# Kernel optimization log

Measured on AMD Instinct MI355X. Metric: run time of the kernel, lower is better.

Reference implementation:

```python
import jax, jax.numpy as jnp
import numpy as np

N = 50000
E = 800000
IN_C = 128
HID = 32
HEADS = 4
G = 512      # number of graphs in batch
OUT_C = 100
NEG_SLOPE = 0.2
EPS = 1e-16


def _gat_params(key, f_in, heads, c):
    k1, k2, k3, k4 = jax.random.split(key, 4)
    s = 1.0 / np.sqrt(f_in)
    return {
        'W': jax.random.uniform(k1, (heads * c, f_in), jnp.float32, -s, s),
        'att_src': jax.random.normal(k2, (heads, c), jnp.float32) * 0.1,
        'att_dst': jax.random.normal(k3, (heads, c), jnp.float32) * 0.1,
        'b': jnp.zeros((heads * c,), jnp.float32),
    }


def setup_inputs() -> dict:
    key = jax.random.key(0)
    ks = jax.random.split(key, 8)
    x = jax.random.normal(ks[0], (N, IN_C), jnp.float32)
    edge_index = jax.random.randint(ks[1], (2, E), 0, N, jnp.int64)
    batch = jnp.sort(jax.random.randint(ks[2], (N,), 0, G, jnp.int64))
    p1 = _gat_params(ks[3], IN_C, HEADS, HID)
    p2 = _gat_params(ks[4], HEADS * HID, HEADS, HID)
    p3 = _gat_params(ks[5], HEADS * HID, HEADS, HID)
    s = 1.0 / np.sqrt(HEADS * HID)
    fc_W = jax.random.uniform(ks[6], (OUT_C, HEADS * HID), jnp.float32, -s, s)
    fc_b = jnp.zeros((OUT_C,), jnp.float32)
    return {
        'x': x, 'edge_index': edge_index, 'batch': batch,
        'W1': p1['W'], 'as1': p1['att_src'], 'ad1': p1['att_dst'], 'b1': p1['b'],
        'W2': p2['W'], 'as2': p2['att_src'], 'ad2': p2['att_dst'], 'b2': p2['b'],
        'W3': p3['W'], 'as3': p3['att_src'], 'ad3': p3['att_dst'], 'b3': p3['b'],
        'fc_W': fc_W, 'fc_b': fc_b,
    }


def gat_conv(x, src, dst, W, att_src, att_dst, b):
    # x: [N, F_in] -> h: [N, H, C]
    h = (x @ W.T).reshape(N, HEADS, HID)
    a_src = jnp.einsum('nhc,hc->nh', h, att_src)   # [N, H]
    a_dst = jnp.einsum('nhc,hc->nh', h, att_dst)
    alpha = a_src[src] + a_dst[dst]                 # [E', H]
    alpha = jax.nn.leaky_relu(alpha, NEG_SLOPE)
    # segment softmax over incoming edges of each dst node
    m = jax.ops.segment_max(alpha, dst, num_segments=N)
    alpha = jnp.exp(alpha - m[dst])
    denom = jax.ops.segment_sum(alpha, dst, num_segments=N)
    alpha = alpha / (denom[dst] + EPS)
    msg = alpha[:, :, None] * h[src]                # [E', H, C]
    out = jax.ops.segment_sum(msg, dst, num_segments=N)
    return out.reshape(N, HEADS * HID) + b


def reference(x, edge_index, batch,
              W1, as1, ad1, b1, W2, as2, ad2, b2, W3, as3, ad3, b3,
              fc_W, fc_b):
    # add self loops (PyG GATConv default)
    loops = jnp.arange(N, dtype=edge_index.dtype)
    src = jnp.concatenate([edge_index[0], loops])
    dst = jnp.concatenate([edge_index[1], loops])
    h = jax.nn.elu(gat_conv(x, src, dst, W1, as1, ad1, b1))
    h = jax.nn.elu(gat_conv(h, src, dst, W2, as2, ad2, b2))
    h = jax.nn.elu(gat_conv(h, src, dst, W3, as3, ad3, b3))
    # global mean pool over graphs
    sums = jax.ops.segment_sum(h, batch, num_segments=G)        # [G, H*C]
    cnts = jax.ops.segment_sum(jnp.ones((N,), h.dtype), batch, num_segments=G)
    pooled = sums / jnp.maximum(cnts, 1.0)[:, None]
    # dropout p=0.5 is identity in eval mode
    return pooled @ fc_W.T + fc_b
```

## Files before the change

### kernel.cpp

```cpp
#include <hip/hip_runtime.h>
#include <math.h>

#define NN 50000
#define EE 800000
#define GG 512
#define OUTC 100
#define NEG 0.2f
#define STRIDE 64
#define SCAT_BLOCKS 782

typedef __attribute__((ext_vector_type(8))) short bf16x8;
typedef __attribute__((ext_vector_type(8))) short s16x8;
typedef __attribute__((ext_vector_type(8))) unsigned short us8;
typedef __attribute__((ext_vector_type(4))) float f32x4;

__device__ inline ushort f2bf(float v) {
  unsigned u = __float_as_uint(v);
  unsigned r = (u + 0x7fff + ((u >> 16) & 1)) >> 16;
  return (ushort)r;
}

__global__ __launch_bounds__(256) void k_scatter_prep(const int* __restrict__ ei,
    int* __restrict__ cursor, ushort* __restrict__ srcs,
    const float* __restrict__ W0, const float* __restrict__ W1, const float* __restrict__ W2,
    const float* __restrict__ as0, const float* __restrict__ as1, const float* __restrict__ as2,
    const float* __restrict__ ad0, const float* __restrict__ ad1, const float* __restrict__ ad2,
    ushort* __restrict__ hi, ushort* __restrict__ lo) {
  if (blockIdx.x < SCAT_BLOCKS) {
    int base = blockIdx.x << 10;
#pragma unroll
    for (int t = 0; t < 4; ++t) {
      int e = base + (t << 8) + threadIdx.x;
      if (e < EE) {
        int d = ei[EE + e];
        int s = ei[e];
        int pos = atomicAdd(&cursor[d], 1);
        if (pos < STRIDE) srcs[(d << 6) + pos] = (ushort)s;
      }
    }
  } else {
    int pb = blockIdx.x - SCAT_BLOCKS;
    int layer = pb / 68, bx = pb % 68;
    const float* W  = (layer == 0) ? W0 : (layer == 1) ? W1 : W2;
    const float* av = (layer == 0) ? as0 : (layer == 1) ? as1 : as2;
    const float* dv = (layer == 0) ? ad0 : (layer == 1) ? ad1 : ad2;
    ushort* hiL = hi + (size_t)layer * 144 * 128;
    ushort* loL = lo + (size_t)layer * 144 * 128;
    int idx = bx * 256 + threadIdx.x;
    if (bx < 64) {
      float v = W[idx];
      ushort hb = f2bf(v);
      float hf = __uint_as_float(((unsigned)hb) << 16);
      hiL[idx] = hb;
      loL[idx] = f2bf(v - hf);
    } else {
      int j2 = idx - 64 * 256;
      int j = j2 >> 7, k = j2 & 127;
      int head = j & 3;
      const float* vec = (j < 4) ? &av[head * 32] : &dv[head * 32];
      float dot = 0.f;
#pragma unroll
      for (int c = 0; c < 32; c++) dot += W[(head * 32 + c) * 128 + k] * vec[c];
      ushort hb = f2bf(dot);
      float hf = __uint_as_float(((unsigned)hb) << 16);
      hiL[(128 + j) * 128 + k] = hb;
      loL[(128 + j) * 128 + k] = f2bf(dot - hf);
      hiL[(136 + j) * 128 + k] = 0;
      loL[(136 + j) * 128 + k] = 0;
    }
  }
}

template <bool TAIL>
__device__ __forceinline__ void gemm_core(const float* __restrict__ feat,
    const ushort* __restrict__ Whi, const ushort* __restrict__ Wlo,
    short* __restrict__ hq, float* __restrict__ asp,
    float* __restrict__ adstf, int n0, int t) {
  int wave = t >> 6, lane = t & 63;
  int quad = lane >> 4, r16 = lane & 15;

  f32x4 acc[2][9];
#pragma unroll
  for (int mt = 0; mt < 2; mt++)
#pragma unroll
    for (int nt = 0; nt < 9; nt++) acc[mt][nt] = (f32x4)0.f;

#pragma unroll
  for (int ks = 0; ks < 4; ks++) {
    bf16x8 ah[2], al[2];
#pragma unroll
    for (int mt = 0; mt < 2; mt++) {
      int row = n0 + wave * 32 + mt * 16 + r16;
      float4 va, vb;
      if (TAIL && row >= NN) {
        va = make_float4(0.f, 0.f, 0.f, 0.f); vb = va;
      } else {
        const float4* fp = (const float4*)&feat[(size_t)row * 128 + ks * 32 + quad * 8];
        va = fp[0]; vb = fp[1];
      }
      float vv[8] = {va.x, va.y, va.z, va.w, vb.x, vb.y, vb.z, vb.w};
      us8 hh, ll;
#pragma unroll
      for (int j = 0; j < 8; j++) {
        ushort hb = f2bf(vv[j]);
        float hf = __uint_as_float(((unsigned)hb) << 16);
        hh[j] = hb;
        ll[j] = (ushort)(__float_as_uint(vv[j] - hf) >> 16);
      }
      ah[mt] = (bf16x8)hh;
      al[mt] = (bf16x8)ll;
    }
#pragma unroll
    for (int nt = 0; nt < 9; nt++) {
      int wrow = (nt < 8) ? (nt * 16 + r16) : (128 + r16);
      size_t wo = (size_t)wrow * 128 + ks * 32 + quad * 8;
      bf16x8 bh = *(const bf16x8*)&Whi[wo];
      bf16x8 bl = *(const bf16x8*)&Wlo[wo];
#pragma unroll
      for (int mt = 0; mt < 2; mt++) {
        acc[mt][nt] = __builtin_amdgcn_mfma_f32_16x16x32_bf16(ah[mt], bh, acc[mt][nt], 0, 0, 0);
        acc[mt][nt] = __builtin_amdgcn_mfma_f32_16x16x32_bf16(al[mt], bh, acc[mt][nt], 0, 0, 0);
        acc[mt][nt] = __builtin_amdgcn_mfma_f32_16x16x32_bf16(ah[mt], bl, acc[mt][nt], 0, 0, 0);
      }
    }
  }

#pragma unroll
  for (int mt = 0; mt < 2; mt++) {
#pragma unroll
    for (int reg = 0; reg < 4; reg++) {
      float am = 0.f;
#pragma unroll
      for (int nt = 0; nt < 8; nt++) am = fmaxf(am, fabsf(acc[mt][nt][reg]));
#pragma unroll
      for (int off = 1; off < 16; off <<= 1) am = fmaxf(am, __shfl_xor(am, off));
      int node = n0 + wave * 32 + mt * 16 + quad * 4 + reg;
      if (!TAIL || node < NN) {
        float amc = fmaxf(am, 1e-20f);
        float rq = 32767.f / amc;
        if (r16 < 4) asp[node * 8 + r16] = acc[mt][8][reg];
        else if (r16 < 8) adstf[node * 4 + r16 - 4] = acc[mt][8][reg];
        else if (r16 == 8) asp[node * 8 + 4] = amc * (1.f / 32767.f);
        short* dq = &hq[(size_t)node * 128 + r16];
#pragma unroll
        for (int nt = 0; nt < 8; nt++)
          dq[nt * 16] = (short)__float2int_rn(acc[mt][nt][reg] * rq);
      }
    }
  }
}

__global__ __launch_bounds__(256) void k_gemm_mfma(const float* __restrict__ feat,
    const ushort* __restrict__ Whi, const ushort* __restrict__ Wlo,
    short* __restrict__ hq, float* __restrict__ asp,
    float* __restrict__ adstf) {
  int n0 = blockIdx.x * 128;
  if (n0 + 128 <= NN)
    gemm_core<false>(feat, Whi, Wlo, hq, asp, adstf, n0, threadIdx.x);
  else
    gemm_core<true>(feat, Whi, Wlo, hq, asp, adstf, n0, threadIdx.x);
}

__global__ __launch_bounds__(256) void k_gather(const short* __restrict__ hq,
    const float* __restrict__ asp,
    const float4* __restrict__ adst,
    const int* __restrict__ cursor, const ushort* __restrict__ srcs,
    const float* __restrict__ bias, float* __restrict__ outf) {
  __shared__ alignas(16) int   s_src[2][4][4][16];
  __shared__ alignas(16) float s_wt[2][4][4][4][20];

  int wave = threadIdx.x >> 6, lane = threadIdx.x & 63;
  int grp = lane >> 4;
  int gl = lane & 15;
  int node = blockIdx.x * 16 + wave * 4 + grp;
  int head = gl >> 2;
  int c0 = gl << 3;

  int deg = 0, e0 = 0;
  float4 ad = make_float4(0.f, 0.f, 0.f, 0.f);
  if (node < NN) {
    deg = min(cursor[node], STRIDE);
    e0 = node << 6;
    ad = adst[node];
  }
  int rounds = (deg + 15) >> 4;

  float acc[8];
#pragma unroll
  for (int i = 0; i < 8; i++) acc[i] = 0.f;
  float ws0 = 0.f, ws1 = 0.f, ws2 = 0.f, ws3 = 0.f;
  float wself = 0.f;

  int nsn = 0, nlive = 0;

  auto phase1 = [&](int r) {
    int j = (r << 4) + gl;
    nlive = (j < deg);
    nsn = nlive ? (int)srcs[e0 + j] : 0;
  };

  auto phase2 = [&](int b) {
    float q0 = 0.f, q1 = 0.f, q2 = 0.f, q3 = 0.f;
    if (nlive) {
      const float4 a = *(const float4*)&asp[nsn * 8];
      float sc = asp[nsn * 8 + 4];
      float v, w0, w1, w2, w3;
      v = a.x + ad.x; v = v > 0.f ? v : NEG * v; w0 = __expf(v);
      v = a.y + ad.y; v = v > 0.f ? v : NEG * v; w1 = __expf(v);
      v = a.z + ad.z; v = v > 0.f ? v : NEG * v; w2 = __expf(v);
      v = a.w + ad.w; v = v > 0.f ? v : NEG * v; w3 = __expf(v);
      ws0 += w0; ws1 += w1; ws2 += w2; ws3 += w3;
      q0 = w0 * sc; q1 = w1 * sc; q2 = w2 * sc; q3 = w3 * sc;
    }
    s_src[b][wave][grp][gl] = nsn << 7;
    s_wt[b][wave][grp][0][gl] = q0;
    s_wt[b][wave][grp][1][gl] = q1;
    s_wt[b][wave][grp][2][gl] = q2;
    s_wt[b][wave][grp][3][gl] = q3;
  };

  auto consume = [&](int r, int b) {
    int cnt = deg - (r << 4);
    cnt = min(cnt, 16);
    const int* srow = &s_src[b][wave][grp][0];
    const float* wrow = &s_wt[b][wave][grp][head][0];
#pragma unroll
    for (int c = 0; c < 2; ++c) {
      int k0 = c << 3;
      if (k0 < cnt) {
        int4 sa = *(const int4*)&srow[k0];
        int4 sb = *(const int4*)&srow[k0 + 4];
        float4 wa = *(const float4*)&wrow[k0];
        float4 wb = *(const float4*)&wrow[k0 + 4];
        s16x8 qa = *(const s16x8*)&hq[sa.x + c0];
        s16x8 qb = *(const s16x8*)&hq[sa.y + c0];
        s16x8 qc = *(const s16x8*)&hq[sa.z + c0];
        s16x8 qd = *(const s16x8*)&hq[sa.w + c0];
        s16x8 qe = *(const s16x8*)&hq[sb.x + c0];
        s16x8 qf = *(const s16x8*)&hq[sb.y + c0];
        s16x8 qg = *(const s16x8*)&hq[sb.z + c0];
        s16x8 qh = *(const s16x8*)&hq[sb.w + c0];
#pragma unroll
        for (int i = 0; i < 8; i++) acc[i] = fmaf(wa.x, (float)qa[i], acc[i]);
#pragma unroll
        for (int i = 0; i < 8; i++) acc[i] = fmaf(wa.y, (float)qb[i], acc[i]);
#pragma unroll
        for (int i = 0; i < 8; i++) acc[i] = fmaf(wa.z, (float)qc[i], acc[i]);
#pragma unroll
        for (int i = 0; i < 8; i++) acc[i] = fmaf(wa.w, (float)qd[i], acc[i]);
        if (k0 + 4 < cnt) {
#pragma unroll
          for (int i = 0; i < 8; i++) acc[i] = fmaf(wb.x, (float)qe[i], acc[i]);
#pragma unroll
          for (int i = 0; i < 8; i++) acc[i] = fmaf(wb.y, (float)qf[i], acc[i]);
#pragma unroll
          for (int i = 0; i < 8; i++) acc[i] = fmaf(wb.z, (float)qg[i], acc[i]);
#pragma unroll
          for (int i = 0; i < 8; i++) acc[i] = fmaf(wb.w, (float)qh[i], acc[i]);
        }
      }
    }
  };

  phase1(0);

  if (node < NN) {
    const float4 a = *(const float4*)&asp[node * 8];
    float sc = asp[node * 8 + 4];
    float v, w0, w1, w2, w3;
    v = a.x + ad.x; v = v > 0.f ? v : NEG * v; w0 = __expf(v);
    v = a.y + ad.y; v = v > 0.f ? v : NEG * v; w1 = __expf(v);
    v = a.z + ad.z; v = v > 0.f ? v : NEG * v; w2 = __expf(v);
    v = a.w + ad.w; v = v > 0.f ? v : NEG * v; w3 = __expf(v);
    float wh = (head == 0) ? w0 : (head == 1) ? w1 : (head == 2) ? w2 : w3;
    wself = wh;
    float wssc = wh * sc;
    s16x8 qs = *(const s16x8*)&hq[(node << 7) + c0];
#pragma unroll
    for (int i = 0; i < 8; i++) acc[i] = wssc * (float)qs[i];
  }

  if (rounds > 0) {
    phase2(0);
    for (int r = 0; r < rounds; ++r) {
      int b = r & 1;
      if (r + 1 < rounds) phase1(r + 1);
      consume(r, b);
      if (r + 1 < rounds) phase2(b ^ 1);
    }
  }

#pragma unroll
  for (int off = 1; off < 16; off <<= 1) {
    ws0 += __shfl_xor(ws0, off);
    ws1 += __shfl_xor(ws1, off);
    ws2 += __shfl_xor(ws2, off);
    ws3 += __shfl_xor(ws3, off);
  }

  if (node < NN) {
    float wsum = wself + ((head == 0) ? ws0 : (head == 1) ? ws1 : (head == 2) ? ws2 : ws3);
    float rcp = 1.f / (wsum + 1e-16f);
    float4 bv0 = *(const float4*)&bias[c0];
    float4 bv1 = *(const float4*)&bias[c0 + 4];
    float bb[8] = {bv0.x, bv0.y, bv0.z, bv0.w, bv1.x, bv1.y, bv1.z, bv1.w};
    float o[8];
#pragma unroll
    for (int i = 0; i < 8; i++) {
      float v = acc[i] * rcp + bb[i];
      o[i] = v > 0.f ? v : expm1f(v);
    }
    *(float4*)&outf[(size_t)node * 128 + c0] = make_float4(o[0], o[1], o[2], o[3]);
    *(float4*)&outf[(size_t)node * 128 + c0 + 4] = make_float4(o[4], o[5], o[6], o[7]);
  }
}

__global__ __launch_bounds__(128) void k_pool(const float* __restrict__ feat,
    const int* __restrict__ batch, float* __restrict__ pooled, float* __restrict__ cnt) {
  int n0 = blockIdx.x * 32;
  int c = threadIdx.x;
  float acc = 0.f; int curg = -1;
  for (int i = 0; i < 32; i++) {
    int n = n0 + i;
    if (n >= NN) break;
    int g = batch[n];
    if (g != curg) {
      if (curg >= 0) atomicAdd(&pooled[curg * 128 + c], acc);
      acc = 0.f; curg = g;
    }
    acc += feat[n * 128 + c];
  }
  if (curg >= 0) atomicAdd(&pooled[curg * 128 + c], acc);
  if (threadIdx.x == 0) {
    float cc = 0.f; int cg = -1;
    for (int i = 0; i < 32; i++) {
      int n = n0 + i;
      if (n >= NN) break;
      int g = batch[n];
      if (g != cg) { if (cg >= 0) atomicAdd(&cnt[cg], cc); cc = 0.f; cg = g; }
      cc += 1.f;
    }
    if (cg >= 0) atomicAdd(&cnt[cg], cc);
  }
}

__global__ __launch_bounds__(128) void k_fc(const float* __restrict__ pooled,
    const float* __restrict__ cnt, const float* __restrict__ fcW,
    const float* __restrict__ fcb, float* __restrict__ out) {
  int g = blockIdx.x;
  __shared__ float p[128];
  int t = threadIdx.x;
  float inv = 1.0f / fmaxf(cnt[g], 1.0f);
  p[t] = pooled[g * 128 + t] * inv;
  __syncthreads();
  if (t < OUTC) {
    float acc = fcb[t];
    const float4* wr = (const float4*)&fcW[t * 128];
    const float4* pp = (const float4*)p;
#pragma unroll
    for (int i = 0; i < 32; i++) {
      float4 w = wr[i], pv = pp[i];
      acc = fmaf(w.x, pv.x, fmaf(w.y, pv.y, fmaf(w.z, pv.z, fmaf(w.w, pv.w, acc))));
    }
    out[g * OUTC + t] = acc;
  }
}

extern "C" void kernel_launch(void* const* d_in, const int* in_sizes, int n_in,
                              void* d_out, int out_size, void* d_ws, size_t ws_size,
                              hipStream_t stream) {
  const float* x    = (const float*)d_in[0];
  const int*   ei   = (const int*)d_in[1];
  const int*   batch= (const int*)d_in[2];
  const float* W1   = (const float*)d_in[3];
  const float* as1  = (const float*)d_in[4];
  const float* ad1  = (const float*)d_in[5];
  const float* b1   = (const float*)d_in[6];
  const float* W2   = (const float*)d_in[7];
  const float* as2  = (const float*)d_in[8];
  const float* ad2  = (const float*)d_in[9];
  const float* b2   = (const float*)d_in[10];
  const float* W3   = (const float*)d_in[11];
  const float* as3  = (const float*)d_in[12];
  const float* ad3  = (const float*)d_in[13];
  const float* b3   = (const float*)d_in[14];
  const float* fcW  = (const float*)d_in[15];
  const float* fcb  = (const float*)d_in[16];
  float* out = (float*)d_out;

  char* p = (char*)d_ws;
  auto alloc = [&](size_t bytes) { char* r = p; p += (bytes + 255) & ~(size_t)255; return r; };
  short* hq     = (short*)alloc((size_t)NN * 128 * 2);
  float* asp    = (float*)alloc((size_t)NN * 8 * 4);
  float* buf0   = (float*)alloc((size_t)NN * 128 * 4);
  float* adstv  = (float*)alloc((size_t)NN * 4 * 4);
  char*  zbase  = p;
  int*   cursor = (int*)alloc((size_t)NN * 4);
  float* pooled = (float*)alloc((size_t)GG * 128 * 4);
  float* cnt    = (float*)alloc((size_t)GG * 4);
  size_t zlen   = (size_t)(p - zbase);
  ushort* srcs  = (ushort*)alloc((size_t)NN * STRIDE * 2);
  ushort* whi   = (ushort*)alloc((size_t)3 * 144 * 128 * 2);
  ushort* wlo   = (ushort*)alloc((size_t)3 * 144 * 128 * 2);

  hipMemsetAsync(zbase, 0, zlen, stream);

  k_scatter_prep<<<SCAT_BLOCKS + 204, 256, 0, stream>>>(ei, cursor, srcs,
      W1, W2, W3, as1, as2, as3, ad1, ad2, ad3, whi, wlo);

  const float* bs[3] = {b1, b2, b3};
  const float* fin = x;
  for (int l = 0; l < 3; l++) {
    k_gemm_mfma<<<(NN + 127) / 128, 256, 0, stream>>>(fin,
        whi + (size_t)l * 144 * 128, wlo + (size_t)l * 144 * 128,
        hq, asp, adstv);
    k_gather<<<(NN + 15) / 16, 256, 0, stream>>>(hq, asp,
        (const float4*)adstv, cursor, srcs, bs[l], buf0);
    fin = buf0;
  }
  k_pool<<<(NN + 31) / 32, 128, 0, stream>>>(buf0, batch, pooled, cnt);
  k_fc<<<GG, 128, 0, stream>>>(pooled, cnt, fcW, fcb, out);
}
```

Before: 375.9 us.

## Fuse edge scatter with layer-1 GEMM and partition scatter by destination range

New measurement: 344.1 us. -8.5%, faster.

```diff
diff --git a/kernel.cpp b/kernel.cpp
--- a/kernel.cpp
+++ b/kernel.cpp
@@ -7,7 +7,11 @@
 #define OUTC 100
 #define NEG 0.2f
 #define STRIDE 64
-#define SCAT_BLOCKS 782
+#define NPART 8
+#define PRNG (NN / NPART)
+#define PCHUNK 4096
+#define SCAT_BLOCKS (NPART * 196)
+#define GEMM_BLOCKS 392
 
 typedef __attribute__((ext_vector_type(8))) short bf16x8;
 typedef __attribute__((ext_vector_type(8))) short s16x8;
@@ -20,54 +24,38 @@
   return (ushort)r;
 }
 
-__global__ __launch_bounds__(256) void k_scatter_prep(const int* __restrict__ ei,
-    int* __restrict__ cursor, ushort* __restrict__ srcs,
+__global__ __launch_bounds__(256) void k_prep(
     const float* __restrict__ W0, const float* __restrict__ W1, const float* __restrict__ W2,
     const float* __restrict__ as0, const float* __restrict__ as1, const float* __restrict__ as2,
     const float* __restrict__ ad0, const float* __restrict__ ad1, const float* __restrict__ ad2,
     ushort* __restrict__ hi, ushort* __restrict__ lo) {
-  if (blockIdx.x < SCAT_BLOCKS) {
-    int base = blockIdx.x << 10;
-#pragma unroll
-    for (int t = 0; t < 4; ++t) {
-      int e = base + (t << 8) + threadIdx.x;
-      if (e < EE) {
-        int d = ei[EE + e];
-        int s = ei[e];
-        int pos = atomicAdd(&cursor[d], 1);
-        if (pos < STRIDE) srcs[(d << 6) + pos] = (ushort)s;
-      }
-    }
+  int layer = blockIdx.x / 68, bx = blockIdx.x % 68;
+  const float* W  = (layer == 0) ? W0 : (layer == 1) ? W1 : W2;
+  const float* av = (layer == 0) ? as0 : (layer == 1) ? as1 : as2;
+  const float* dv = (layer == 0) ? ad0 : (layer == 1) ? ad1 : ad2;
+  ushort* hiL = hi + (size_t)layer * 144 * 128;
+  ushort* loL = lo + (size_t)layer * 144 * 128;
+  int idx = bx * 256 + threadIdx.x;
+  if (bx < 64) {
+    float v = W[idx];
+    ushort hb = f2bf(v);
+    float hf = __uint_as_float(((unsigned)hb) << 16);
+    hiL[idx] = hb;
+    loL[idx] = f2bf(v - hf);
   } else {
-    int pb = blockIdx.x - SCAT_BLOCKS;
-    int layer = pb / 68, bx = pb % 68;
-    const float* W  = (layer == 0) ? W0 : (layer == 1) ? W1 : W2;
-    const float* av = (layer == 0) ? as0 : (layer == 1) ? as1 : as2;
-    const float* dv = (layer == 0) ? ad0 : (layer == 1) ? ad1 : ad2;
-    ushort* hiL = hi + (size_t)layer * 144 * 128;
-    ushort* loL = lo + (size_t)layer * 144 * 128;
-    int idx = bx * 256 + threadIdx.x;
-    if (bx < 64) {
-      float v = W[idx];
-      ushort hb = f2bf(v);
-      float hf = __uint_as_float(((unsigned)hb) << 16);
-      hiL[idx] = hb;
-      loL[idx] = f2bf(v - hf);
-    } else {
-      int j2 = idx - 64 * 256;
-      int j = j2 >> 7, k = j2 & 127;
-      int head = j & 3;
-      const float* vec = (j < 4) ? &av[head * 32] : &dv[head * 32];
-      float dot = 0.f;
-#pragma unroll
-      for (int c = 0; c < 32; c++) dot += W[(head * 32 + c) * 128 + k] * vec[c];
-      ushort hb = f2bf(dot);
-      float hf = __uint_as_float(((unsigned)hb) << 16);
-      hiL[(128 + j) * 128 + k] = hb;
-      loL[(128 + j) * 128 + k] = f2bf(dot - hf);
-      hiL[(136 + j) * 128 + k] = 0;
-      loL[(136 + j) * 128 + k] = 0;
-    }
+    int j2 = idx - 64 * 256;
+    int j = j2 >> 7, k = j2 & 127;
+    int head = j & 3;
+    const float* vec = (j < 4) ? &av[head * 32] : &dv[head * 32];
+    float dot = 0.f;
+#pragma unroll
+    for (int c = 0; c < 32; c++) dot += W[(head * 32 + c) * 128 + k] * vec[c];
+    ushort hb = f2bf(dot);
+    float hf = __uint_as_float(((unsigned)hb) << 16);
+    hiL[(128 + j) * 128 + k] = hb;
+    loL[(128 + j) * 128 + k] = f2bf(dot - hf);
+    hiL[(136 + j) * 128 + k] = 0;
+    loL[(136 + j) * 128 + k] = 0;
   }
 }
 
@@ -159,6 +147,43 @@
     gemm_core<false>(feat, Whi, Wlo, hq, asp, adstf, n0, threadIdx.x);
   else
     gemm_core<true>(feat, Whi, Wlo, hq, asp, adstf, n0, threadIdx.x);
+}
+
+__global__ __launch_bounds__(256) void k_fused(const float* __restrict__ feat,
+    const ushort* __restrict__ Whi, const ushort* __restrict__ Wlo,
+    short* __restrict__ hq, float* __restrict__ asp, float* __restrict__ adstf,
+    const int* __restrict__ ei, int* __restrict__ cursor, ushort* __restrict__ srcs) {
+  if (blockIdx.x < GEMM_BLOCKS) {
+    int n0 = blockIdx.x * 128;
+    if (n0 >= NN) return;
+    if (n0 + 128 <= NN)
+      gemm_core<false>(feat, Whi, Wlo, hq, asp, adstf, n0, threadIdx.x);
+    else
+      gemm_core<true>(feat, Whi, Wlo, hq, asp, adstf, n0, threadIdx.x);
+    return;
+  }
+  int sb = blockIdx.x - GEMM_BLOCKS;
+  int part = sb & (NPART - 1);
+  int chunk = sb >> 3;
+  int plo = part * PRNG, phi = plo + PRNG;
+  int base = chunk * PCHUNK;
+#pragma unroll
+  for (int it = 0; it < PCHUNK / 1024; ++it) {
+    int e = base + it * 1024 + (threadIdx.x << 2);
+    if (e >= EE) break;
+    int4 d4 = *(const int4*)&ei[EE + e];
+    bool m0 = (d4.x >= plo) & (d4.x < phi);
+    bool m1 = (d4.y >= plo) & (d4.y < phi);
+    bool m2 = (d4.z >= plo) & (d4.z < phi);
+    bool m3 = (d4.w >= plo) & (d4.w < phi);
+    if (m0 | m1 | m2 | m3) {
+      int4 s4 = *(const int4*)&ei[e];
+      if (m0) { int p = atomicAdd(&cursor[d4.x], 1); if (p < STRIDE) srcs[(d4.x << 6) + p] = (ushort)s4.x; }
+      if (m1) { int p = atomicAdd(&cursor[d4.y], 1); if (p < STRIDE) srcs[(d4.y << 6) + p] = (ushort)s4.y; }
+      if (m2) { int p = atomicAdd(&cursor[d4.z], 1); if (p < STRIDE) srcs[(d4.z << 6) + p] = (ushort)s4.z; }
+      if (m3) { int p = atomicAdd(&cursor[d4.w], 1); if (p < STRIDE) srcs[(d4.w << 6) + p] = (ushort)s4.w; }
+    }
+  }
 }
 
 __global__ __launch_bounds__(256) void k_gather(const short* __restrict__ hq,
@@ -405,18 +430,20 @@
 
   hipMemsetAsync(zbase, 0, zlen, stream);
 
-  k_scatter_prep<<<SCAT_BLOCKS + 204, 256, 0, stream>>>(ei, cursor, srcs,
-      W1, W2, W3, as1, as2, as3, ad1, ad2, ad3, whi, wlo);
+  k_prep<<<204, 256, 0, stream>>>(W1, W2, W3, as1, as2, as3, ad1, ad2, ad3, whi, wlo);
+
+  k_fused<<<GEMM_BLOCKS + SCAT_BLOCKS, 256, 0, stream>>>(x, whi, wlo,
+      hq, asp, adstv, ei, cursor, srcs);
+  k_gather<<<(NN + 15) / 16, 256, 0, stream>>>(hq, asp,
+      (const float4*)adstv, cursor, srcs, b1, buf0);
 
   const float* bs[3] = {b1, b2, b3};
-  const float* fin = x;
-  for (int l = 0; l < 3; l++) {
-    k_gemm_mfma<<<(NN + 127) / 128, 256, 0, stream>>>(fin,
+  for (int l = 1; l < 3; l++) {
+    k_gemm_mfma<<<(NN + 127) / 128, 256, 0, stream>>>(buf0,
         whi + (size_t)l * 144 * 128, wlo + (size_t)l * 144 * 128,
         hq, asp, adstv);
     k_gather<<<(NN + 15) / 16, 256, 0, stream>>>(hq, asp,
         (const float4*)adstv, cursor, srcs, bs[l], buf0);
-    fin = buf0;
   }
   k_pool<<<(NN + 31) / 32, 128, 0, stream>>>(buf0, batch, pooled, cnt);
   k_fc<<<GG, 128, 0, stream>>>(pooled, cnt, fcW, fcb, out);
```

## Partition edge scatter by destination range and halve GEMM rows per wave

Applied to the files above, without the earlier changes.

Measured after the change: 395.4 us. 5.2% more time.

```diff
diff --git a/kernel.cpp b/kernel.cpp
--- a/kernel.cpp
+++ b/kernel.cpp
@@ -7,7 +7,11 @@
 #define OUTC 100
 #define NEG 0.2f
 #define STRIDE 64
-#define SCAT_BLOCKS 782
+#define NPART 8
+#define PRNG (NN / NPART)
+#define PCHUNK 4096
+#define NCHUNK 196
+#define SCAT_BLOCKS (NPART * NCHUNK)
 
 typedef __attribute__((ext_vector_type(8))) short bf16x8;
 typedef __attribute__((ext_vector_type(8))) short s16x8;
@@ -27,15 +31,34 @@
     const float* __restrict__ ad0, const float* __restrict__ ad1, const float* __restrict__ ad2,
     ushort* __restrict__ hi, ushort* __restrict__ lo) {
   if (blockIdx.x < SCAT_BLOCKS) {
-    int base = blockIdx.x << 10;
-#pragma unroll
-    for (int t = 0; t < 4; ++t) {
-      int e = base + (t << 8) + threadIdx.x;
-      if (e < EE) {
-        int d = ei[EE + e];
-        int s = ei[e];
-        int pos = atomicAdd(&cursor[d], 1);
-        if (pos < STRIDE) srcs[(d << 6) + pos] = (ushort)s;
+    int part = blockIdx.x & (NPART - 1);
+    int chunk = blockIdx.x >> 3;
+    int plo = part * PRNG, phi = plo + PRNG;
+    int base = chunk * PCHUNK + (threadIdx.x << 2);
+    int4 d[4];
+    bool lv[4];
+#pragma unroll
+    for (int it = 0; it < 4; ++it) {
+      int e = base + (it << 10);
+      lv[it] = (e < EE);
+      if (lv[it]) d[it] = *(const int4*)&ei[EE + e];
+      else        d[it] = make_int4(-1, -1, -1, -1);
+    }
+#pragma unroll
+    for (int it = 0; it < 4; ++it) {
+      if (!lv[it]) continue;
+      int e = base + (it << 10);
+      int4 dd = d[it];
+      bool m0 = (dd.x >= plo) & (dd.x < phi);
+      bool m1 = (dd.y >= plo) & (dd.y < phi);
+      bool m2 = (dd.z >= plo) & (dd.z < phi);
+      bool m3 = (dd.w >= plo) & (dd.w < phi);
+      if (m0 | m1 | m2 | m3) {
+        int4 s4 = *(const int4*)&ei[e];
+        if (m0) { int p = atomicAdd(&cursor[dd.x], 1); if (p < STRIDE) srcs[(dd.x << 6) + p] = (ushort)s4.x; }
+        if (m1) { int p = atomicAdd(&cursor[dd.y], 1); if (p < STRIDE) srcs[(dd.y << 6) + p] = (ushort)s4.y; }
+        if (m2) { int p = atomicAdd(&cursor[dd.z], 1); if (p < STRIDE) srcs[(dd.z << 6) + p] = (ushort)s4.z; }
+        if (m3) { int p = atomicAdd(&cursor[dd.w], 1); if (p < STRIDE) srcs[(dd.w << 6) + p] = (ushort)s4.w; }
       }
     }
   } else {
@@ -78,24 +101,21 @@
     float* __restrict__ adstf, int n0, int t) {
   int wave = t >> 6, lane = t & 63;
   int quad = lane >> 4, r16 = lane & 15;
-
-  f32x4 acc[2][9];
-#pragma unroll
-  for (int mt = 0; mt < 2; mt++)
-#pragma unroll
-    for (int nt = 0; nt < 9; nt++) acc[mt][nt] = (f32x4)0.f;
+  int rowA = n0 + wave * 16 + r16;
+
+  f32x4 acc[9];
+#pragma unroll
+  for (int nt = 0; nt < 9; nt++) acc[nt] = (f32x4)0.f;
 
 #pragma unroll
   for (int ks = 0; ks < 4; ks++) {
-    bf16x8 ah[2], al[2];
-#pragma unroll
-    for (int mt = 0; mt < 2; mt++) {
-      int row = n0 + wave * 32 + mt * 16 + r16;
+    bf16x8 ah, al;
+    {
       float4 va, vb;
-      if (TAIL && row >= NN) {
+      if (TAIL && rowA >= NN) {
         va = make_float4(0.f, 0.f, 0.f, 0.f); vb = va;
       } else {
-        const float4* fp = (const float4*)&feat[(size_t)row * 128 + ks * 32 + quad * 8];
+        const float4* fp = (const float4*)&feat[(size_t)rowA * 128 + ks * 32 + quad * 8];
         va = fp[0]; vb = fp[1];
       }
       float vv[8] = {va.x, va.y, va.z, va.w, vb.x, vb.y, vb.z, vb.w};
@@ -107,8 +127,8 @@
         hh[j] = hb;
         ll[j] = (ushort)(__float_as_uint(vv[j] - hf) >> 16);
       }
-      ah[mt] = (bf16x8)hh;
-      al[mt] = (bf16x8)ll;
+      ah = (bf16x8)hh;
+      al = (bf16x8)ll;
     }
 #pragma unroll
     for (int nt = 0; nt < 9; nt++) {
@@ -116,36 +136,30 @@
       size_t wo = (size_t)wrow * 128 + ks * 32 + quad * 8;
       bf16x8 bh = *(const bf16x8*)&Whi[wo];
       bf16x8 bl = *(const bf16x8*)&Wlo[wo];
-#pragma unroll
-      for (int mt = 0; mt < 2; mt++) {
-        acc[mt][nt] = __builtin_amdgcn_mfma_f32_16x16x32_bf16(ah[mt], bh, acc[mt][nt], 0, 0, 0);
-        acc[mt][nt] = __builtin_amdgcn_mfma_f32_16x16x32_bf16(al[mt], bh, acc[mt][nt], 0, 0, 0);
-        acc[mt][nt] = __builtin_amdgcn_mfma_f32_16x16x32_bf16(ah[mt], bl, acc[mt][nt], 0, 0, 0);
-      }
-    }
-  }
-
-#pragma unroll
-  for (int mt = 0; mt < 2; mt++) {
-#pragma unroll
-    for (int reg = 0; reg < 4; reg++) {
-      float am = 0.f;
-#pragma unroll
-      for (int nt = 0; nt < 8; nt++) am = fmaxf(am, fabsf(acc[mt][nt][reg]));
-#pragma unroll
-      for (int off = 1; off < 16; off <<= 1) am = fmaxf(am, __shfl_xor(am, off));
-      int node = n0 + wave * 32 + mt * 16 + quad * 4 + reg;
-      if (!TAIL || node < NN) {
-        float amc = fmaxf(am, 1e-20f);
-        float rq = 32767.f / amc;
-        if (r16 < 4) asp[node * 8 + r16] = acc[mt][8][reg];
-        else if (r16 < 8) adstf[node * 4 + r16 - 4] = acc[mt][8][reg];
-        else if (r16 == 8) asp[node * 8 + 4] = amc * (1.f / 32767.f);
-        short* dq = &hq[(size_t)node * 128 + r16];
-#pragma unroll
-        for (int nt = 0; nt < 8; nt++)
-          dq[nt * 16] = (short)__float2int_rn(acc[mt][nt][reg] * rq);
-      }
+      acc[nt] = __builtin_amdgcn_mfma_f32_16x16x32_bf16(ah, bh, acc[nt], 0, 0, 0);
+      acc[nt] = __builtin_amdgcn_mfma_f32_16x16x32_bf16(al, bh, acc[nt], 0, 0, 0);
+      acc[nt] = __builtin_amdgcn_mfma_f32_16x16x32_bf16(ah, bl, acc[nt], 0, 0, 0);
+    }
+  }
+
+#pragma unroll
+  for (int reg = 0; reg < 4; reg++) {
+    float am = 0.f;
+#pragma unroll
+    for (int nt = 0; nt < 8; nt++) am = fmaxf(am, fabsf(acc[nt][reg]));
+#pragma unroll
+    for (int off = 1; off < 16; off <<= 1) am = fmaxf(am, __shfl_xor(am, off));
+    int node = n0 + wave * 16 + quad * 4 + reg;
+    if (!TAIL || node < NN) {
+      float amc = fmaxf(am, 1e-20f);
+      float rq = 32767.f / amc;
+      if (r16 < 4) asp[node * 8 + r16] = acc[8][reg];
+      else if (r16 < 8) adstf[node * 4 + r16 - 4] = acc[8][reg];
+      else if (r16 == 8) asp[node * 8 + 4] = amc * (1.f / 32767.f);
+      short* dq = &hq[(size_t)node * 128 + r16];
+#pragma unroll
+      for (int nt = 0; nt < 8; nt++)
+        dq[nt * 16] = (short)__float2int_rn(acc[nt][reg] * rq);
     }
   }
 }
@@ -154,8 +168,8 @@
     const ushort* __restrict__ Whi, const ushort* __restrict__ Wlo,
     short* __restrict__ hq, float* __restrict__ asp,
     float* __restrict__ adstf) {
-  int n0 = blockIdx.x * 128;
-  if (n0 + 128 <= NN)
+  int n0 = blockIdx.x * 64;
+  if (n0 + 64 <= NN)
     gemm_core<false>(feat, Whi, Wlo, hq, asp, adstf, n0, threadIdx.x);
   else
     gemm_core<true>(feat, Whi, Wlo, hq, asp, adstf, n0, threadIdx.x);
@@ -411,7 +425,7 @@
   const float* bs[3] = {b1, b2, b3};
   const float* fin = x;
   for (int l = 0; l < 3; l++) {
-    k_gemm_mfma<<<(NN + 127) / 128, 256, 0, stream>>>(fin,
+    k_gemm_mfma<<<(NN + 63) / 64, 256, 0, stream>>>(fin,
         whi + (size_t)l * 144 * 128, wlo + (size_t)l * 144 * 128,
         hq, asp, adstv);
     k_gather<<<(NN + 15) / 16, 256, 0, stream>>>(hq, asp,
```
